# Performance work log

Measured on AMD Instinct MI355X. Metric: run time of the kernel, lower is better.

## Reference

```python
import jax, jax.numpy as jnp
import numpy as np

S_MUL, V_MUL = 32, 16          # 32x0e + 16x1o
NODE_DIM = S_MUL + 3 * V_MUL   # 80
LATENT = 128
INV_SQRT3 = 1.0 / np.sqrt(3.0)          # wigner 3j (1,1,0) / (0,1,1) / (1,0,1) factor
C_SCALAR = np.float32(1.0 / np.sqrt(48.0))   # path_norm 'element': fan into 0e = 32*1 + 16*1
C_VECTOR = np.float32(np.sqrt(3.0 / 48.0))   # irrep dim 3 / fan 48 for 1o output


def setup_inputs() -> dict:
    rng = np.random.default_rng(0)
    B, n_atoms, radius = 2048, 32, 5.0
    N = B * n_atoms
    # atoms uniform in a 10A cube -> ~300 edges per 32-atom graph at r=5
    pos_g = rng.uniform(0.0, 10.0, size=(B, n_atoms, 3)).astype(np.float32)
    diff = pos_g[:, :, None, :] - pos_g[:, None, :, :]
    d2 = (diff * diff).sum(-1)
    mask = (d2 <= radius * radius) & (d2 > 0.0)   # same predicate as build_radius_graph
    b_idx, i_idx, j_idx = np.nonzero(mask)
    edge_index = np.stack([b_idx * n_atoms + i_idx, b_idx * n_atoms + j_idx]).astype(np.int32)
    pos = pos_g.reshape(N, 3)
    z = rng.integers(0, 100, size=N).astype(np.int32)
    batch = np.repeat(np.arange(B, dtype=np.int32), n_atoms)
    L = 3  # num_layers

    def w(*shape, scale=1.0):
        return jnp.asarray((rng.standard_normal(shape) * scale).astype(np.float32))

    return dict(
        pos=jnp.asarray(pos), z=jnp.asarray(z), batch=jnp.asarray(batch),
        edge_index=jnp.asarray(edge_index), num_graphs=B,
        emb=w(100, S_MUL),                      # nn.Embedding(100, 32) ~ N(0,1)
        W_s2n=w(S_MUL, S_MUL),                  # e3nn Linear 32x0e -> 32x0e path
        W1=w(L, S_MUL, S_MUL),                  # tp path 0e x 0e -> 0e
        W2=w(L, S_MUL, V_MUL),                  # tp path 0e x 1o -> 1o
        W3=w(L, V_MUL, V_MUL),                  # tp path 1o x 0e -> 1o
        W4=w(L, V_MUL, S_MUL),                  # tp path 1o x 1o -> 0e
        Ws=w(L, S_MUL, S_MUL),                  # e3nn Linear scalar block
        Wv=w(L, V_MUL, V_MUL),                  # e3nn Linear vector block
        Wr1=w(NODE_DIM, 256, scale=1.0 / np.sqrt(NODE_DIM)), br1=jnp.zeros((256,), jnp.float32),
        Wr2=w(256, LATENT, scale=1.0 / np.sqrt(256.0)), br2=jnp.zeros((LATENT,), jnp.float32),
    )


def _forward(pos, emb, W_s2n, W1, W2, W3, W4, Ws, Wv, Wr1, br1, Wr2, br2,
             z, batch, edge_index, num_graphs):
    N = pos.shape[0]
    src, dst = edge_index[0], edge_index[1]
    # atom embedding -> node irreps (only 0e->0e path exists; vectors start at 0)
    s = (emb[z] @ W_s2n) * np.float32(1.0 / np.sqrt(S_MUL))   # (N, 32)
    v = jnp.zeros((N, V_MUL, 3), pos.dtype)                   # (N, 16, 3)
    # spherical harmonics, normalize=True, 'component': Y0 = 1, Y1 = sqrt(3) * r_hat
    rij = pos[dst] - pos[src]                                 # (E, 3)
    sh1 = np.float32(np.sqrt(3.0)) * rij / jnp.linalg.norm(rij, axis=-1, keepdims=True)
    for l in range(W1.shape[0]):
        ss, vs = s[src], v[src]                               # gather (E,32), (E,16,3)
        # FullyConnectedTensorProduct(node, sh, node), uvw weights, sh0 == 1
        m_s = C_SCALAR * (jnp.einsum('eu,uw->ew', ss, W1[l])
                          + INV_SQRT3 * jnp.einsum('eui,ei,uw->ew', vs, sh1, W4[l]))
        m_v = (C_VECTOR * INV_SQRT3) * (jnp.einsum('eu,ei,uw->ewi', ss, sh1, W2[l])
                                        + jnp.einsum('eui,uw->ewi', vs, W3[l]))
        a_s = jax.ops.segment_sum(m_s, dst, num_segments=N)   # index_add_ scatter
        a_v = jax.ops.segment_sum(m_v, dst, num_segments=N)
        # e3nn Linear (per-irrep block, 1/sqrt(fan_in)) then relu on FULL feature (as in source)
        h_s = jax.nn.relu((a_s @ Ws[l]) * np.float32(1.0 / np.sqrt(S_MUL)))
        h_v = jax.nn.relu(jnp.einsum('nvi,vw->nwi', a_v, Wv[l]) * np.float32(1.0 / np.sqrt(V_MUL)))
        s, v = s + h_s, v + h_v                               # residual
    x = jnp.concatenate([s, v.reshape(N, V_MUL * 3)], axis=-1)  # (N, 80)
    hg = jax.ops.segment_sum(x, batch, num_segments=num_graphs) # sum-pool per graph
    return jax.nn.relu(hg @ Wr1 + br1) @ Wr2 + br2              # (B, latent)


def reference(pos, emb, W_s2n, W1, W2, W3, W4, Ws, Wv, Wr1, br1, Wr2, br2,
              z, batch, edge_index, num_graphs):
    return _forward(pos, emb, W_s2n, W1, W2, W3, W4, Ws, Wv, Wr1, br1, Wr2, br2,
                    z, batch, edge_index, num_graphs)
```

## Files before the change

### kernel.cpp

```cpp
#include <hip/hip_runtime.h>
#include <math.h>

typedef __attribute__((ext_vector_type(8))) short bf16x8;
typedef __attribute__((ext_vector_type(4))) float f32x4;

#define SQRT3F     1.7320508075688772f
#define SCALE_T    0.17677669529663687f
#define SCALE_M1   0.025515518153991442f
#define SCALE_M2   0.014731391274719739f
#define SCALE_M34  0.036084391824351615f

#define FSTR 40
#define ASTR 72

__device__ __forceinline__ ushort f2bf(float f) {
    union { float f; unsigned u; } v; v.f = f;
    unsigned u = v.u;
    return (ushort)((u + 0x7FFFu + ((u >> 16) & 1u)) >> 16);
}
__device__ __forceinline__ float bf2f(ushort h) {
    union { unsigned u; float f; } v; v.u = ((unsigned)h) << 16;
    return v.f;
}
__device__ __forceinline__ f32x4 mfma(bf16x8 a, bf16x8 b, f32x4 c) {
    return __builtin_amdgcn_mfma_f32_16x16x32_bf16(a, b, c, 0, 0, 0);
}
__device__ __forceinline__ void storeAgg(ushort* AG, f32x4 t, int u0, int n) {
    uint2 u;
    u.x = f2bf(t[0]) | ((unsigned)f2bf(t[1]) << 16);
    u.y = f2bf(t[2]) | ((unsigned)f2bf(t[3]) << 16);
    *(uint2*)&AG[n*ASTR + u0] = u;
}
__device__ __forceinline__ void rmw4(ushort* F, int c, int n0, f32x4 h) {
    uint2* p = (uint2*)&F[c*FSTR + n0];
    uint2 o = *p;
    float f0 = bf2f((ushort)(o.x      )) + fmaxf(h[0], 0.f);
    float f1 = bf2f((ushort)(o.x >> 16)) + fmaxf(h[1], 0.f);
    float f2 = bf2f((ushort)(o.y      )) + fmaxf(h[2], 0.f);
    float f3 = bf2f((ushort)(o.y >> 16)) + fmaxf(h[3], 0.f);
    uint2 w;
    w.x = f2bf(f0) | ((unsigned)f2bf(f1) << 16);
    w.y = f2bf(f2) | ((unsigned)f2bf(f3) << 16);
    *p = w;
}

__global__ void prep_kernel(const float* __restrict__ emb,
                            const float* __restrict__ W_s2n,
                            const float* __restrict__ W1, const float* __restrict__ W2,
                            const float* __restrict__ W3, const float* __restrict__ W4,
                            const float* __restrict__ Ws, const float* __restrict__ Wv,
                            ushort* __restrict__ Tbf, ushort* __restrict__ Mbf)
{
    int idx = blockIdx.x * blockDim.x + threadIdx.x;
    if (idx < 3200) {
        int r = idx >> 5, c = idx & 31;
        float acc = 0.f;
        for (int k = 0; k < 32; ++k) acc += emb[r*32 + k] * W_s2n[k*32 + c];
        Tbf[idx] = f2bf(acc * SCALE_T);
        return;
    }
    idx -= 3200;
    if (idx < 3*48*64) {
        int lyr = idx / 3072, rem = idx % 3072;
        int row = rem >> 6, u = rem & 63;
        float val = 0.f;
        if (row < 32) {
            int w = row;
            if (u < 32) {
                float a = 0.f;
                for (int k = 0; k < 32; ++k)
                    a += W1[lyr*1024 + u*32 + k] * Ws[lyr*1024 + k*32 + w];
                val = a * SCALE_M1;
            } else if (u < 48) {
                int uu = u - 32; float a = 0.f;
                for (int k = 0; k < 32; ++k)
                    a += W4[lyr*512 + uu*32 + k] * Ws[lyr*1024 + k*32 + w];
                val = a * SCALE_M2;
            }
        } else {
            int w = row - 32;
            if (u < 32) {
                float a = 0.f;
                for (int k = 0; k < 16; ++k)
                    a += W2[lyr*512 + u*16 + k] * Wv[lyr*256 + k*16 + w];
                val = a * SCALE_M34;
            } else if (u < 48) {
                int uu = u - 32; float a = 0.f;
                for (int k = 0; k < 16; ++k)
                    a += W3[lyr*256 + uu*16 + k] * Wv[lyr*256 + k*16 + w];
                val = a * SCALE_M34;
            }
        }
        Mbf[lyr*3072 + row*64 + u] = f2bf(val);
    }
}

__global__ __launch_bounds__(256)
void gnn_kernel(const float* __restrict__ pos, const int* __restrict__ z,
                const ushort* __restrict__ Tbf, const ushort* __restrict__ Mbf,
                const float* __restrict__ Wr1, const float* __restrict__ br1,
                const float* __restrict__ Wr2, const float* __restrict__ br2,
                float* __restrict__ out, int B)
{
    __shared__ __align__(16) char smem[45312];
    ushort* featA = (ushort*)smem;
    ushort* aggA  = (ushort*)(smem + 25600);
    float*  hgl   = (float*)(smem + 44032);
    float*  h1    = (float*)aggA;
    float*  red   = ((float*)aggA) + 1024;

    const int tid = threadIdx.x;
    const int wv = tid >> 6, l = tid & 63;
    const int g  = blockIdx.x*4 + wv;
    ushort* F  = featA + wv*80*FSTR;
    ushort* AG = aggA  + wv*32*ASTR;

    for (int i = l; i < 32*(ASTR/2); i += 64) ((uint*)AG)[i] = 0;
    for (int i = l; i < 48*(FSTR/2); i += 64) ((uint*)(F + 32*FSTR))[i] = 0;

    {
        int n = l & 31, h = l >> 5;
        int zg = z[g*32 + n];
        uint4 t0 = *(const uint4*)(Tbf + zg*32 + h*16);
        uint4 t1 = *(const uint4*)(Tbf + zg*32 + h*16 + 8);
        unsigned ua[8] = {t0.x, t0.y, t0.z, t0.w, t1.x, t1.y, t1.z, t1.w};
        #pragma unroll
        for (int q = 0; q < 8; ++q) {
            F[(h*16 + 2*q    )*FSTR + n] = (ushort)ua[q];
            F[(h*16 + 2*q + 1)*FSTR + n] = (ushort)(ua[q] >> 16);
        }
    }

    const int ln = l & 15, kq = l >> 4;
    bf16x8 adjf[4][2];
    {
        const int k0 = kq*8;
        #pragma unroll
        for (int nt = 0; nt < 2; ++nt) {
            int ng = g*32 + nt*16 + ln;
            float px = pos[3*ng], py = pos[3*ng+1], pz = pos[3*ng+2];
            union { bf16x8 v; ushort s[8]; } o[4];
            #pragma unroll
            for (int jj = 0; jj < 8; ++jj) {
                int j = g*32 + k0 + jj;
                float dx = __fsub_rn(px, pos[3*j]);
                float dy = __fsub_rn(py, pos[3*j+1]);
                float dz = __fsub_rn(pz, pos[3*j+2]);
                float d2 = __fadd_rn(__fadd_rn(__fmul_rn(dx,dx), __fmul_rn(dy,dy)),
                                     __fmul_rn(dz,dz));
                bool on = (d2 <= 25.0f) && (d2 > 0.0f);
                float rinv = on ? rsqrtf(d2) * SQRT3F : 0.f;
                o[0].s[jj] = on ? (ushort)0x3F80 : (ushort)0;
                o[1].s[jj] = f2bf(dx * rinv);
                o[2].s[jj] = f2bf(dy * rinv);
                o[3].s[jj] = f2bf(dz * rinv);
            }
            #pragma unroll
            for (int w = 0; w < 4; ++w) adjf[w][nt] = o[w].v;
        }
    }

    const f32x4 z4 = {0.f, 0.f, 0.f, 0.f};

    for (int lay = 0; lay < 3; ++lay) {
        const ushort* Mg = Mbf + lay*3072;
        bf16x8 fs0 = *(const bf16x8*)&F[(     ln)*FSTR + kq*8];
        bf16x8 fs1 = *(const bf16x8*)&F[(16 + ln)*FSTR + kq*8];
        bf16x8 fv0 = *(const bf16x8*)&F[(32 + ln)*FSTR + kq*8];
        bf16x8 fv1 = *(const bf16x8*)&F[(48 + ln)*FSTR + kq*8];
        bf16x8 fv2 = *(const bf16x8*)&F[(64 + ln)*FSTR + kq*8];
        bf16x8 bmS0[2], bmS1[2], bmV[2];
        #pragma unroll
        for (int kc = 0; kc < 2; ++kc) {
            bmS0[kc] = *(const bf16x8*)&Mg[(     ln)*64 + kc*32 + kq*8];
            bmS1[kc] = *(const bf16x8*)&Mg[(16 + ln)*64 + kc*32 + kq*8];
            bmV [kc] = *(const bf16x8*)&Mg[(32 + ln)*64 + kc*32 + kq*8];
        }

        #pragma unroll
        for (int nt = 0; nt < 2; ++nt) {
            f32x4 t;
            t = mfma(fs0, adjf[0][nt], z4);
            storeAgg(AG, t,      kq*4, nt*16 + ln);
            t = mfma(fs1, adjf[0][nt], z4);
            storeAgg(AG, t, 16 + kq*4, nt*16 + ln);
            t = mfma(fv2, adjf[3][nt], z4);
            t = mfma(fv1, adjf[2][nt], t);
            t = mfma(fv0, adjf[1][nt], t);
            storeAgg(AG, t, 32 + kq*4, nt*16 + ln);
        }
        f32x4 hs[2][2] = {{z4, z4}, {z4, z4}};
        #pragma unroll
        for (int kc = 0; kc < 2; ++kc)
            #pragma unroll
            for (int mt = 0; mt < 2; ++mt) {
                bf16x8 ag = *(const bf16x8*)&AG[(mt*16 + ln)*ASTR + kc*32 + kq*8];
                hs[mt][0] = mfma(ag, bmS0[kc], hs[mt][0]);
                hs[mt][1] = mfma(ag, bmS1[kc], hs[mt][1]);
            }
        #pragma unroll
        for (int mt = 0; mt < 2; ++mt)
            #pragma unroll
            for (int wt = 0; wt < 2; ++wt)
                rmw4(F, wt*16 + ln, mt*16 + kq*4, hs[mt][wt]);

        #pragma unroll
        for (int i = 0; i < 3; ++i) {
            bf16x8 fvi = (i == 0) ? fv0 : (i == 1) ? fv1 : fv2;
            #pragma unroll
            for (int nt = 0; nt < 2; ++nt) {
                f32x4 t;
                t = mfma(fs0, adjf[1+i][nt], z4);
                storeAgg(AG, t,      kq*4, nt*16 + ln);
                t = mfma(fs1, adjf[1+i][nt], z4);
                storeAgg(AG, t, 16 + kq*4, nt*16 + ln);
                t = mfma(fvi, adjf[0][nt], z4);
                storeAgg(AG, t, 32 + kq*4, nt*16 + ln);
            }
            f32x4 hv[2] = {z4, z4};
            #pragma unroll
            for (int kc = 0; kc < 2; ++kc)
                #pragma unroll
                for (int mt = 0; mt < 2; ++mt) {
                    bf16x8 ag = *(const bf16x8*)&AG[(mt*16 + ln)*ASTR + kc*32 + kq*8];
                    hv[mt] = mfma(ag, bmV[kc], hv[mt]);
                }
            #pragma unroll
            for (int mt = 0; mt < 2; ++mt)
                rmw4(F, 32 + i*16 + ln, mt*16 + kq*4, hv[mt]);
        }
    }

    for (int f = l; f < 80; f += 64) {
        const ushort* row;
        if (f < 32) row = &F[f*FSTR];
        else { int c = f - 32, w = c/3, i = c - 3*w; row = &F[(32 + i*16 + w)*FSTR]; }
        const uint* r32 = (const uint*)row;
        float acc = 0.f;
        #pragma unroll
        for (int q = 0; q < 16; ++q) {
            uint u = r32[q];
            acc += bf2f((ushort)u) + bf2f((ushort)(u >> 16));
        }
        hgl[wv*80 + f] = acc;
    }
    __syncthreads();

    {
        const int w = tid;
        float acc0 = br1[w];
        float acc1 = acc0, acc2 = acc0, acc3 = acc0;
        #pragma unroll 4
        for (int f = 0; f < 80; ++f) {
            float wvv = Wr1[f*256 + w];
            acc0 = fmaf(hgl[0*80 + f], wvv, acc0);
            acc1 = fmaf(hgl[1*80 + f], wvv, acc1);
            acc2 = fmaf(hgl[2*80 + f], wvv, acc2);
            acc3 = fmaf(hgl[3*80 + f], wvv, acc3);
        }
        h1[0*256 + w] = fmaxf(acc0, 0.f);
        h1[1*256 + w] = fmaxf(acc1, 0.f);
        h1[2*256 + w] = fmaxf(acc2, 0.f);
        h1[3*256 + w] = fmaxf(acc3, 0.f);
    }
    __syncthreads();
    {
        const int g0 = blockIdx.x * 4;
        const int w2 = tid & 127, kh = tid >> 7;
        const float4* h1v = (const float4*)h1;
        float s0 = 0.f, s1 = 0.f, s2 = 0.f, s3 = 0.f;
        #pragma unroll 2
        for (int k4 = kh*32; k4 < kh*32 + 32; ++k4) {
            float4 hA = h1v[0*64 + k4];
            float4 hB = h1v[1*64 + k4];
            float4 hC = h1v[2*64 + k4];
            float4 hD = h1v[3*64 + k4];
            int k = k4 * 4;
            float m0 = Wr2[(size_t)(k+0)*128 + w2];
            float m1 = Wr2[(size_t)(k+1)*128 + w2];
            float m2 = Wr2[(size_t)(k+2)*128 + w2];
            float m3 = Wr2[(size_t)(k+3)*128 + w2];
            s0 = fmaf(hA.x,m0, fmaf(hA.y,m1, fmaf(hA.z,m2, fmaf(hA.w,m3, s0))));
            s1 = fmaf(hB.x,m0, fmaf(hB.y,m1, fmaf(hB.z,m2, fmaf(hB.w,m3, s1))));
            s2 = fmaf(hC.x,m0, fmaf(hC.y,m1, fmaf(hC.z,m2, fmaf(hC.w,m3, s2))));
            s3 = fmaf(hD.x,m0, fmaf(hD.y,m1, fmaf(hD.z,m2, fmaf(hD.w,m3, s3))));
        }
        if (kh) {
            red[0*128 + w2] = s0; red[1*128 + w2] = s1;
            red[2*128 + w2] = s2; red[3*128 + w2] = s3;
        }
        __syncthreads();
        if (!kh) {
            float b = br2[w2];
            out[(size_t)(g0+0)*128 + w2] = s0 + red[0*128 + w2] + b;
            out[(size_t)(g0+1)*128 + w2] = s1 + red[1*128 + w2] + b;
            out[(size_t)(g0+2)*128 + w2] = s2 + red[2*128 + w2] + b;
            out[(size_t)(g0+3)*128 + w2] = s3 + red[3*128 + w2] + b;
        }
    }
}

extern "C" void kernel_launch(void* const* d_in, const int* in_sizes, int n_in,
                              void* d_out, int out_size, void* d_ws, size_t ws_size,
                              hipStream_t stream)
{
    const float* pos   = (const float*)d_in[0];
    const int*   z     = (const int*)d_in[1];
    const float* emb   = (const float*)d_in[5];
    const float* W_s2n = (const float*)d_in[6];
    const float* W1    = (const float*)d_in[7];
    const float* W2    = (const float*)d_in[8];
    const float* W3    = (const float*)d_in[9];
    const float* W4    = (const float*)d_in[10];
    const float* Ws    = (const float*)d_in[11];
    const float* Wv    = (const float*)d_in[12];
    const float* Wr1   = (const float*)d_in[13];
    const float* br1   = (const float*)d_in[14];
    const float* Wr2   = (const float*)d_in[15];
    const float* br2   = (const float*)d_in[16];
    float* out = (float*)d_out;

    const int B = out_size / 128;

    char* p = (char*)d_ws;
    ushort* Tbf = (ushort*)p;  p += 6400;
    ushort* Mbf = (ushort*)p;  p += 18432;

    const int prep_total = 3200 + 3*48*64;
    prep_kernel<<<(prep_total + 255) / 256, 256, 0, stream>>>(
        emb, W_s2n, W1, W2, W3, W4, Ws, Wv, Tbf, Mbf);

    gnn_kernel<<<B / 4, 256, 0, stream>>>(pos, z, Tbf, Mbf,
                                          Wr1, br1, Wr2, br2, out, B);
}
```

Baseline: 113.6 us.

## Split each graph across two wavefronts, doubling block size to 512 threads

Each graph's 32 nodes are now handled by two wavefronts, each owning 16 node rows, instead of one wavefront per graph. The block grows to 512 threads while still covering four graphs, and the readout MLP is re-split so each thread does fewer graphs. The aim is more wavefronts in flight to hide latency and less per-wave serial MFMA work. In exchange, __syncthreads barriers are added inside the layer loop because the two wavefronts share feature rows, and shared-memory-bound occupancy may limit the benefit.

```diff
diff --git a/kernel.cpp b/kernel.cpp
--- a/kernel.cpp
+++ b/kernel.cpp
@@ -95,7 +95,7 @@
     }
 }
 
-__global__ __launch_bounds__(256)
+__global__ __launch_bounds__(512, 4)
 void gnn_kernel(const float* __restrict__ pos, const int* __restrict__ z,
                 const ushort* __restrict__ Tbf, const ushort* __restrict__ Mbf,
                 const float* __restrict__ Wr1, const float* __restrict__ br1,
@@ -107,60 +107,65 @@
     ushort* aggA  = (ushort*)(smem + 25600);
     float*  hgl   = (float*)(smem + 44032);
     float*  h1    = (float*)aggA;
-    float*  red   = ((float*)aggA) + 1024;
 
     const int tid = threadIdx.x;
     const int wv = tid >> 6, l = tid & 63;
-    const int g  = blockIdx.x*4 + wv;
-    ushort* F  = featA + wv*80*FSTR;
-    ushort* AG = aggA  + wv*32*ASTR;
-
-    for (int i = l; i < 32*(ASTR/2); i += 64) ((uint*)AG)[i] = 0;
-    for (int i = l; i < 48*(FSTR/2); i += 64) ((uint*)(F + 32*FSTR))[i] = 0;
-
-    {
-        int n = l & 31, h = l >> 5;
+    const int wg = wv >> 1, r = wv & 1;
+    const int g  = blockIdx.x*4 + wg;
+    ushort* F  = featA + wg*80*FSTR;
+    ushort* AG = aggA  + wg*32*ASTR;
+
+    {
+        #pragma unroll
+        for (int t2 = 0; t2 < 2; ++t2) {
+            int i = t2*64 + l;
+            int row = r*16 + (i >> 3);
+            ((uint*)AG)[row*36 + 24 + (i & 7)] = 0;
+        }
+    }
+    for (int i = l; i < 480; i += 64)
+        ((uint*)(F + 32*FSTR))[r*480 + i] = 0;
+
+    {
+        int n = r*16 + (l & 15), h = l >> 4;
         int zg = z[g*32 + n];
-        uint4 t0 = *(const uint4*)(Tbf + zg*32 + h*16);
-        uint4 t1 = *(const uint4*)(Tbf + zg*32 + h*16 + 8);
-        unsigned ua[8] = {t0.x, t0.y, t0.z, t0.w, t1.x, t1.y, t1.z, t1.w};
-        #pragma unroll
-        for (int q = 0; q < 8; ++q) {
-            F[(h*16 + 2*q    )*FSTR + n] = (ushort)ua[q];
-            F[(h*16 + 2*q + 1)*FSTR + n] = (ushort)(ua[q] >> 16);
+        uint4 t0 = *(const uint4*)(Tbf + zg*32 + h*8);
+        unsigned ua[4] = {t0.x, t0.y, t0.z, t0.w};
+        #pragma unroll
+        for (int q = 0; q < 4; ++q) {
+            F[(h*8 + 2*q    )*FSTR + n] = (ushort)ua[q];
+            F[(h*8 + 2*q + 1)*FSTR + n] = (ushort)(ua[q] >> 16);
         }
     }
 
     const int ln = l & 15, kq = l >> 4;
-    bf16x8 adjf[4][2];
+    bf16x8 adjf[4];
     {
         const int k0 = kq*8;
-        #pragma unroll
-        for (int nt = 0; nt < 2; ++nt) {
-            int ng = g*32 + nt*16 + ln;
-            float px = pos[3*ng], py = pos[3*ng+1], pz = pos[3*ng+2];
-            union { bf16x8 v; ushort s[8]; } o[4];
-            #pragma unroll
-            for (int jj = 0; jj < 8; ++jj) {
-                int j = g*32 + k0 + jj;
-                float dx = __fsub_rn(px, pos[3*j]);
-                float dy = __fsub_rn(py, pos[3*j+1]);
-                float dz = __fsub_rn(pz, pos[3*j+2]);
-                float d2 = __fadd_rn(__fadd_rn(__fmul_rn(dx,dx), __fmul_rn(dy,dy)),
-                                     __fmul_rn(dz,dz));
-                bool on = (d2 <= 25.0f) && (d2 > 0.0f);
-                float rinv = on ? rsqrtf(d2) * SQRT3F : 0.f;
-                o[0].s[jj] = on ? (ushort)0x3F80 : (ushort)0;
-                o[1].s[jj] = f2bf(dx * rinv);
-                o[2].s[jj] = f2bf(dy * rinv);
-                o[3].s[jj] = f2bf(dz * rinv);
-            }
-            #pragma unroll
-            for (int w = 0; w < 4; ++w) adjf[w][nt] = o[w].v;
-        }
+        int ng = g*32 + r*16 + ln;
+        float px = pos[3*ng], py = pos[3*ng+1], pz = pos[3*ng+2];
+        union { bf16x8 v; ushort s[8]; } o[4];
+        #pragma unroll
+        for (int jj = 0; jj < 8; ++jj) {
+            int j = g*32 + k0 + jj;
+            float dx = __fsub_rn(px, pos[3*j]);
+            float dy = __fsub_rn(py, pos[3*j+1]);
+            float dz = __fsub_rn(pz, pos[3*j+2]);
+            float d2 = __fadd_rn(__fadd_rn(__fmul_rn(dx,dx), __fmul_rn(dy,dy)),
+                                 __fmul_rn(dz,dz));
+            bool on = (d2 <= 25.0f) && (d2 > 0.0f);
+            float rinv = on ? rsqrtf(d2) * SQRT3F : 0.f;
+            o[0].s[jj] = on ? (ushort)0x3F80 : (ushort)0;
+            o[1].s[jj] = f2bf(dx * rinv);
+            o[2].s[jj] = f2bf(dy * rinv);
+            o[3].s[jj] = f2bf(dz * rinv);
+        }
+        #pragma unroll
+        for (int w = 0; w < 4; ++w) adjf[w] = o[w].v;
     }
 
     const f32x4 z4 = {0.f, 0.f, 0.f, 0.f};
+    __syncthreads();
 
     for (int lay = 0; lay < 3; ++lay) {
         const ushort* Mg = Mbf + lay*3072;
@@ -176,62 +181,54 @@
             bmS1[kc] = *(const bf16x8*)&Mg[(16 + ln)*64 + kc*32 + kq*8];
             bmV [kc] = *(const bf16x8*)&Mg[(32 + ln)*64 + kc*32 + kq*8];
         }
-
-        #pragma unroll
-        for (int nt = 0; nt < 2; ++nt) {
+        __syncthreads();
+
+        {
             f32x4 t;
-            t = mfma(fs0, adjf[0][nt], z4);
-            storeAgg(AG, t,      kq*4, nt*16 + ln);
-            t = mfma(fs1, adjf[0][nt], z4);
-            storeAgg(AG, t, 16 + kq*4, nt*16 + ln);
-            t = mfma(fv2, adjf[3][nt], z4);
-            t = mfma(fv1, adjf[2][nt], t);
-            t = mfma(fv0, adjf[1][nt], t);
-            storeAgg(AG, t, 32 + kq*4, nt*16 + ln);
-        }
-        f32x4 hs[2][2] = {{z4, z4}, {z4, z4}};
-        #pragma unroll
-        for (int kc = 0; kc < 2; ++kc)
-            #pragma unroll
-            for (int mt = 0; mt < 2; ++mt) {
-                bf16x8 ag = *(const bf16x8*)&AG[(mt*16 + ln)*ASTR + kc*32 + kq*8];
-                hs[mt][0] = mfma(ag, bmS0[kc], hs[mt][0]);
-                hs[mt][1] = mfma(ag, bmS1[kc], hs[mt][1]);
-            }
-        #pragma unroll
-        for (int mt = 0; mt < 2; ++mt)
-            #pragma unroll
-            for (int wt = 0; wt < 2; ++wt)
-                rmw4(F, wt*16 + ln, mt*16 + kq*4, hs[mt][wt]);
+            t = mfma(fs0, adjf[0], z4);
+            storeAgg(AG, t,      kq*4, r*16 + ln);
+            t = mfma(fs1, adjf[0], z4);
+            storeAgg(AG, t, 16 + kq*4, r*16 + ln);
+            t = mfma(fv2, adjf[3], z4);
+            t = mfma(fv1, adjf[2], t);
+            t = mfma(fv0, adjf[1], t);
+            storeAgg(AG, t, 32 + kq*4, r*16 + ln);
+        }
+        f32x4 hs[2] = {z4, z4};
+        #pragma unroll
+        for (int kc = 0; kc < 2; ++kc) {
+            bf16x8 ag = *(const bf16x8*)&AG[(r*16 + ln)*ASTR + kc*32 + kq*8];
+            hs[0] = mfma(ag, bmS0[kc], hs[0]);
+            hs[1] = mfma(ag, bmS1[kc], hs[1]);
+        }
+        rmw4(F,      ln, r*16 + kq*4, hs[0]);
+        rmw4(F, 16 + ln, r*16 + kq*4, hs[1]);
 
         #pragma unroll
         for (int i = 0; i < 3; ++i) {
             bf16x8 fvi = (i == 0) ? fv0 : (i == 1) ? fv1 : fv2;
+            {
+                f32x4 t;
+                t = mfma(fs0, adjf[1+i], z4);
+                storeAgg(AG, t,      kq*4, r*16 + ln);
+                t = mfma(fs1, adjf[1+i], z4);
+                storeAgg(AG, t, 16 + kq*4, r*16 + ln);
+                t = mfma(fvi, adjf[0], z4);
+                storeAgg(AG, t, 32 + kq*4, r*16 + ln);
+            }
+            f32x4 hv = z4;
             #pragma unroll
-            for (int nt = 0; nt < 2; ++nt) {
-                f32x4 t;
-                t = mfma(fs0, adjf[1+i][nt], z4);
-                storeAgg(AG, t,      kq*4, nt*16 + ln);
-                t = mfma(fs1, adjf[1+i][nt], z4);
-                storeAgg(AG, t, 16 + kq*4, nt*16 + ln);
-                t = mfma(fvi, adjf[0][nt], z4);
-                storeAgg(AG, t, 32 + kq*4, nt*16 + ln);
+            for (int kc = 0; kc < 2; ++kc) {
+                bf16x8 ag = *(const bf16x8*)&AG[(r*16 + ln)*ASTR + kc*32 + kq*8];
+                hv = mfma(ag, bmV[kc], hv);
             }
-            f32x4 hv[2] = {z4, z4};
-            #pragma unroll
-            for (int kc = 0; kc < 2; ++kc)
-                #pragma unroll
-                for (int mt = 0; mt < 2; ++mt) {
-                    bf16x8 ag = *(const bf16x8*)&AG[(mt*16 + ln)*ASTR + kc*32 + kq*8];
-                    hv[mt] = mfma(ag, bmV[kc], hv[mt]);
-                }
-            #pragma unroll
-            for (int mt = 0; mt < 2; ++mt)
-                rmw4(F, 32 + i*16 + ln, mt*16 + kq*4, hv[mt]);
-        }
-    }
-
-    for (int f = l; f < 80; f += 64) {
+            rmw4(F, 32 + i*16 + ln, r*16 + kq*4, hv);
+        }
+        __syncthreads();
+    }
+
+    if (l < 40) {
+        int f = r*40 + l;
         const ushort* row;
         if (f < 32) row = &F[f*FSTR];
         else { int c = f - 32, w = c/3, i = c - 3*w; row = &F[(32 + i*16 + w)*FSTR]; }
@@ -242,61 +239,40 @@
             uint u = r32[q];
             acc += bf2f((ushort)u) + bf2f((ushort)(u >> 16));
         }
-        hgl[wv*80 + f] = acc;
+        hgl[wg*80 + f] = acc;
     }
     __syncthreads();
 
     {
-        const int w = tid;
-        float acc0 = br1[w];
-        float acc1 = acc0, acc2 = acc0, acc3 = acc0;
+        const int w = tid & 255, gh = tid >> 8;
+        float a0 = br1[w], a1 = a0;
+        const float* hg0 = &hgl[(gh*2    )*80];
+        const float* hg1 = &hgl[(gh*2 + 1)*80];
         #pragma unroll 4
         for (int f = 0; f < 80; ++f) {
             float wvv = Wr1[f*256 + w];
-            acc0 = fmaf(hgl[0*80 + f], wvv, acc0);
-            acc1 = fmaf(hgl[1*80 + f], wvv, acc1);
-            acc2 = fmaf(hgl[2*80 + f], wvv, acc2);
-            acc3 = fmaf(hgl[3*80 + f], wvv, acc3);
-        }
-        h1[0*256 + w] = fmaxf(acc0, 0.f);
-        h1[1*256 + w] = fmaxf(acc1, 0.f);
-        h1[2*256 + w] = fmaxf(acc2, 0.f);
-        h1[3*256 + w] = fmaxf(acc3, 0.f);
+            a0 = fmaf(hg0[f], wvv, a0);
+            a1 = fmaf(hg1[f], wvv, a1);
+        }
+        h1[(gh*2    )*256 + w] = fmaxf(a0, 0.f);
+        h1[(gh*2 + 1)*256 + w] = fmaxf(a1, 0.f);
     }
     __syncthreads();
     {
-        const int g0 = blockIdx.x * 4;
-        const int w2 = tid & 127, kh = tid >> 7;
-        const float4* h1v = (const float4*)h1;
-        float s0 = 0.f, s1 = 0.f, s2 = 0.f, s3 = 0.f;
+        const int w2 = tid & 127, gi = tid >> 7;
+        const float4* h1v = (const float4*)&h1[gi*256];
+        float s = 0.f;
         #pragma unroll 2
-        for (int k4 = kh*32; k4 < kh*32 + 32; ++k4) {
-            float4 hA = h1v[0*64 + k4];
-            float4 hB = h1v[1*64 + k4];
-            float4 hC = h1v[2*64 + k4];
-            float4 hD = h1v[3*64 + k4];
+        for (int k4 = 0; k4 < 64; ++k4) {
+            float4 hh = h1v[k4];
             int k = k4 * 4;
             float m0 = Wr2[(size_t)(k+0)*128 + w2];
             float m1 = Wr2[(size_t)(k+1)*128 + w2];
             float m2 = Wr2[(size_t)(k+2)*128 + w2];
             float m3 = Wr2[(size_t)(k+3)*128 + w2];
-            s0 = fmaf(hA.x,m0, fmaf(hA.y,m1, fmaf(hA.z,m2, fmaf(hA.w,m3, s0))));
-            s1 = fmaf(hB.x,m0, fmaf(hB.y,m1, fmaf(hB.z,m2, fmaf(hB.w,m3, s1))));
-            s2 = fmaf(hC.x,m0, fmaf(hC.y,m1, fmaf(hC.z,m2, fmaf(hC.w,m3, s2))));
-            s3 = fmaf(hD.x,m0, fmaf(hD.y,m1, fmaf(hD.z,m2, fmaf(hD.w,m3, s3))));
-        }
-        if (kh) {
-            red[0*128 + w2] = s0; red[1*128 + w2] = s1;
-            red[2*128 + w2] = s2; red[3*128 + w2] = s3;
-        }
-        __syncthreads();
-        if (!kh) {
-            float b = br2[w2];
-            out[(size_t)(g0+0)*128 + w2] = s0 + red[0*128 + w2] + b;
-            out[(size_t)(g0+1)*128 + w2] = s1 + red[1*128 + w2] + b;
-            out[(size_t)(g0+2)*128 + w2] = s2 + red[2*128 + w2] + b;
-            out[(size_t)(g0+3)*128 + w2] = s3 + red[3*128 + w2] + b;
-        }
+            s = fmaf(hh.x,m0, fmaf(hh.y,m1, fmaf(hh.z,m2, fmaf(hh.w,m3, s))));
+        }
+        out[(size_t)(blockIdx.x*4 + gi)*128 + w2] = s + br2[w2];
     }
 }
 
@@ -330,6 +306,6 @@
     prep_kernel<<<(prep_total + 255) / 256, 256, 0, stream>>>(
         emb, W_s2n, W1, W2, W3, W4, Ws, Wv, Tbf, Mbf);
 
-    gnn_kernel<<<B / 4, 256, 0, stream>>>(pos, z, Tbf, Mbf,
+    gnn_kernel<<<B / 4, 512, 0, stream>>>(pos, z, Tbf, Mbf,
                                           Wr1, br1, Wr2, br2, out, B);
 }
```

Result: slower. 116.3 us (+2.4%).

## Fuse weight-folding prep into main kernel via per-block MFMA into LDS

Applied to the files above, without the earlier changes.

Removes the separate prep kernel and instead has every block compute the folded layer matrices (tensor-product weights times linear weights) with MFMA into a swizzled shared-memory buffer. Node embeddings are likewise computed in-kernel by an MFMA of embedding rows with W_s2n. This aims to eliminate a kernel launch and its serialization gap, at the cost of redundant per-block weight computation, extra global reads of fp32 weights, a block-wide barrier, and larger shared memory that may lower occupancy.

```diff
diff --git a/kernel.cpp b/kernel.cpp
--- a/kernel.cpp
+++ b/kernel.cpp
@@ -43,69 +43,25 @@
     w.y = f2bf(f2) | ((unsigned)f2bf(f3) << 16);
     *p = w;
 }
-
-__global__ void prep_kernel(const float* __restrict__ emb,
-                            const float* __restrict__ W_s2n,
-                            const float* __restrict__ W1, const float* __restrict__ W2,
-                            const float* __restrict__ W3, const float* __restrict__ W4,
-                            const float* __restrict__ Ws, const float* __restrict__ Wv,
-                            ushort* __restrict__ Tbf, ushort* __restrict__ Mbf)
-{
-    int idx = blockIdx.x * blockDim.x + threadIdx.x;
-    if (idx < 3200) {
-        int r = idx >> 5, c = idx & 31;
-        float acc = 0.f;
-        for (int k = 0; k < 32; ++k) acc += emb[r*32 + k] * W_s2n[k*32 + c];
-        Tbf[idx] = f2bf(acc * SCALE_T);
-        return;
-    }
-    idx -= 3200;
-    if (idx < 3*48*64) {
-        int lyr = idx / 3072, rem = idx % 3072;
-        int row = rem >> 6, u = rem & 63;
-        float val = 0.f;
-        if (row < 32) {
-            int w = row;
-            if (u < 32) {
-                float a = 0.f;
-                for (int k = 0; k < 32; ++k)
-                    a += W1[lyr*1024 + u*32 + k] * Ws[lyr*1024 + k*32 + w];
-                val = a * SCALE_M1;
-            } else if (u < 48) {
-                int uu = u - 32; float a = 0.f;
-                for (int k = 0; k < 32; ++k)
-                    a += W4[lyr*512 + uu*32 + k] * Ws[lyr*1024 + k*32 + w];
-                val = a * SCALE_M2;
-            }
-        } else {
-            int w = row - 32;
-            if (u < 32) {
-                float a = 0.f;
-                for (int k = 0; k < 16; ++k)
-                    a += W2[lyr*512 + u*16 + k] * Wv[lyr*256 + k*16 + w];
-                val = a * SCALE_M34;
-            } else if (u < 48) {
-                int uu = u - 32; float a = 0.f;
-                for (int k = 0; k < 16; ++k)
-                    a += W3[lyr*256 + uu*16 + k] * Wv[lyr*256 + k*16 + w];
-                val = a * SCALE_M34;
-            }
-        }
-        Mbf[lyr*3072 + row*64 + u] = f2bf(val);
-    }
+__device__ __forceinline__ char* mlPtr(char* ML, int row, int colS) {
+    return ML + (((row * 128) + colS * 2) ^ ((row & 7) << 4));
 }
 
 __global__ __launch_bounds__(256)
 void gnn_kernel(const float* __restrict__ pos, const int* __restrict__ z,
-                const ushort* __restrict__ Tbf, const ushort* __restrict__ Mbf,
+                const float* __restrict__ emb, const float* __restrict__ W_s2n,
+                const float* __restrict__ W1, const float* __restrict__ W2,
+                const float* __restrict__ W3, const float* __restrict__ W4,
+                const float* __restrict__ Ws, const float* __restrict__ Wv,
                 const float* __restrict__ Wr1, const float* __restrict__ br1,
                 const float* __restrict__ Wr2, const float* __restrict__ br2,
-                float* __restrict__ out, int B)
+                float* __restrict__ out)
 {
-    __shared__ __align__(16) char smem[45312];
+    __shared__ __align__(16) char smem[63744];
     ushort* featA = (ushort*)smem;
     ushort* aggA  = (ushort*)(smem + 25600);
-    float*  hgl   = (float*)(smem + 44032);
+    char*   MLb   = smem + 44032;
+    float*  hgl   = (float*)(smem + 62464);
     float*  h1    = (float*)aggA;
     float*  red   = ((float*)aggA) + 1024;
 
@@ -114,24 +70,93 @@
     const int g  = blockIdx.x*4 + wv;
     ushort* F  = featA + wv*80*FSTR;
     ushort* AG = aggA  + wv*32*ASTR;
+    const int ln = l & 15, kq = l >> 4;
+    const f32x4 z4 = {0.f, 0.f, 0.f, 0.f};
 
     for (int i = l; i < 32*(ASTR/2); i += 64) ((uint*)AG)[i] = 0;
     for (int i = l; i < 48*(FSTR/2); i += 64) ((uint*)(F + 32*FSTR))[i] = 0;
+    for (int i = tid; i < 144*8; i += 256) {
+        int row = i >> 3, c = i & 7;
+        *(uint*)(MLb + (((row*128) + 96 + c*4) ^ ((row & 7) << 4))) = 0;
+    }
+
+    for (int t = wv; t < 27; t += 4) {
+        int lay = t / 9, rr = t - lay*9;
+        union { bf16x8 v; ushort s[8]; } af, bfv;
+        int w0, u0;
+        if (rr < 6) {
+            w0 = (rr & 1)*16; u0 = (rr >> 1)*16;
+            #pragma unroll
+            for (int e = 0; e < 8; ++e)
+                af.s[e] = f2bf(Ws[lay*1024 + (kq*8+e)*32 + w0 + ln]);
+            if (u0 < 32) {
+                const float* src = W1 + lay*1024 + (u0+ln)*32 + kq*8;
+                #pragma unroll
+                for (int e = 0; e < 8; ++e) bfv.s[e] = f2bf(src[e] * SCALE_M1);
+            } else {
+                const float* src = W4 + lay*512 + ln*32 + kq*8;
+                #pragma unroll
+                for (int e = 0; e < 8; ++e) bfv.s[e] = f2bf(src[e] * SCALE_M2);
+            }
+        } else {
+            w0 = 32; u0 = (rr - 6)*16;
+            #pragma unroll
+            for (int e = 0; e < 8; ++e) {
+                int k = kq*8 + e;
+                af.s[e] = (k < 16) ? f2bf(Wv[lay*256 + k*16 + ln]) : (ushort)0;
+            }
+            if (u0 < 32) {
+                #pragma unroll
+                for (int e = 0; e < 8; ++e) {
+                    int k = kq*8 + e;
+                    float x = (k < 16) ? W2[lay*512 + (u0+ln)*16 + k] : 0.f;
+                    bfv.s[e] = f2bf(x * SCALE_M34);
+                }
+            } else {
+                #pragma unroll
+                for (int e = 0; e < 8; ++e) {
+                    int k = kq*8 + e;
+                    float x = (k < 16) ? W3[lay*256 + ln*16 + k] : 0.f;
+                    bfv.s[e] = f2bf(x * SCALE_M34);
+                }
+            }
+        }
+        f32x4 d = mfma(af.v, bfv.v, z4);
+        #pragma unroll
+        for (int q = 0; q < 4; ++q) {
+            int row = lay*48 + w0 + kq*4 + q;
+            *(ushort*)mlPtr(MLb, row, u0 + ln) = f2bf(d[q]);
+        }
+    }
 
     {
-        int n = l & 31, h = l >> 5;
-        int zg = z[g*32 + n];
-        uint4 t0 = *(const uint4*)(Tbf + zg*32 + h*16);
-        uint4 t1 = *(const uint4*)(Tbf + zg*32 + h*16 + 8);
-        unsigned ua[8] = {t0.x, t0.y, t0.z, t0.w, t1.x, t1.y, t1.z, t1.w};
-        #pragma unroll
-        for (int q = 0; q < 8; ++q) {
-            F[(h*16 + 2*q    )*FSTR + n] = (ushort)ua[q];
-            F[(h*16 + 2*q + 1)*FSTR + n] = (ushort)(ua[q] >> 16);
-        }
-    }
-
-    const int ln = l & 15, kq = l >> 4;
+        union { bf16x8 v; ushort s[8]; } aT[2], bE[2];
+        #pragma unroll
+        for (int c = 0; c < 2; ++c)
+            #pragma unroll
+            for (int e = 0; e < 8; ++e)
+                aT[c].s[e] = f2bf(W_s2n[(kq*8+e)*32 + c*16 + ln] * SCALE_T);
+        #pragma unroll
+        for (int n = 0; n < 2; ++n) {
+            int zz = z[g*32 + n*16 + ln];
+            const float* er = emb + zz*32 + kq*8;
+            float4 e0 = *(const float4*)er, e1 = *(const float4*)(er + 4);
+            bE[n].s[0] = f2bf(e0.x); bE[n].s[1] = f2bf(e0.y);
+            bE[n].s[2] = f2bf(e0.z); bE[n].s[3] = f2bf(e0.w);
+            bE[n].s[4] = f2bf(e1.x); bE[n].s[5] = f2bf(e1.y);
+            bE[n].s[6] = f2bf(e1.z); bE[n].s[7] = f2bf(e1.w);
+        }
+        #pragma unroll
+        for (int c = 0; c < 2; ++c)
+            #pragma unroll
+            for (int n = 0; n < 2; ++n) {
+                f32x4 d = mfma(aT[c].v, bE[n].v, z4);
+                #pragma unroll
+                for (int q = 0; q < 4; ++q)
+                    F[(c*16 + kq*4 + q)*FSTR + n*16 + ln] = f2bf(d[q]);
+            }
+    }
+
     bf16x8 adjf[4][2];
     {
         const int k0 = kq*8;
@@ -160,10 +185,10 @@
         }
     }
 
-    const f32x4 z4 = {0.f, 0.f, 0.f, 0.f};
+    __syncthreads();
 
     for (int lay = 0; lay < 3; ++lay) {
-        const ushort* Mg = Mbf + lay*3072;
+        const int layRow = lay*48;
         bf16x8 fs0 = *(const bf16x8*)&F[(     ln)*FSTR + kq*8];
         bf16x8 fs1 = *(const bf16x8*)&F[(16 + ln)*FSTR + kq*8];
         bf16x8 fv0 = *(const bf16x8*)&F[(32 + ln)*FSTR + kq*8];
@@ -172,9 +197,9 @@
         bf16x8 bmS0[2], bmS1[2], bmV[2];
         #pragma unroll
         for (int kc = 0; kc < 2; ++kc) {
-            bmS0[kc] = *(const bf16x8*)&Mg[(     ln)*64 + kc*32 + kq*8];
-            bmS1[kc] = *(const bf16x8*)&Mg[(16 + ln)*64 + kc*32 + kq*8];
-            bmV [kc] = *(const bf16x8*)&Mg[(32 + ln)*64 + kc*32 + kq*8];
+            bmS0[kc] = *(const bf16x8*)mlPtr(MLb, layRow +      ln, kc*32 + kq*8);
+            bmS1[kc] = *(const bf16x8*)mlPtr(MLb, layRow + 16 + ln, kc*32 + kq*8);
+            bmV [kc] = *(const bf16x8*)mlPtr(MLb, layRow + 32 + ln, kc*32 + kq*8);
         }
 
         #pragma unroll
@@ -322,14 +347,7 @@
 
     const int B = out_size / 128;
 
-    char* p = (char*)d_ws;
-    ushort* Tbf = (ushort*)p;  p += 6400;
-    ushort* Mbf = (ushort*)p;  p += 18432;
-
-    const int prep_total = 3200 + 3*48*64;
-    prep_kernel<<<(prep_total + 255) / 256, 256, 0, stream>>>(
-        emb, W_s2n, W1, W2, W3, W4, Ws, Wv, Tbf, Mbf);
-
-    gnn_kernel<<<B / 4, 256, 0, stream>>>(pos, z, Tbf, Mbf,
-                                          Wr1, br1, Wr2, br2, out, B);
-}
+    gnn_kernel<<<B / 4, 256, 0, stream>>>(pos, z, emb, W_s2n,
+                                          W1, W2, W3, W4, Ws, Wv,
+                                          Wr1, br1, Wr2, br2, out);
+}
```

Result: slower. 121.2 us (+6.7%).
